# Kernel tuning notes

Hardware: AMD Instinct MI355X
Metric: run time of the kernel (lower is better)

Reference implementation:

```python
import jax, jax.numpy as jnp
import numpy as np

DIM = 512
HEADS = 8
DIM_HEAD = 64
INNER = HEADS * DIM_HEAD  # 512
B, N = 4, 2048


def setup_inputs() -> dict:
    key = jax.random.key(0)
    k1, k2, k3, k4 = jax.random.split(key, 4)
    x = jax.random.normal(k1, (B, N, DIM), dtype=jnp.float32)
    # nn.Linear(dim, inner*3, bias=False): weight [3*inner, dim]; store transposed [dim, 3*inner]
    w_qkv = jax.random.normal(k2, (DIM, 3 * INNER), dtype=jnp.float32) / np.sqrt(DIM)
    w_out = jax.random.normal(k3, (INNER, DIM), dtype=jnp.float32) / np.sqrt(INNER)
    b_out = jax.random.normal(k4, (DIM,), dtype=jnp.float32) * 0.01
    return {"x": x, "w_qkv": w_qkv, "w_out": w_out, "b_out": b_out}


def reference(x, w_qkv, w_out, b_out):
    b, n, _ = x.shape
    scale = DIM_HEAD ** -0.5
    qkv = x @ w_qkv  # [b, n, 3*inner]
    q, k, v = jnp.split(qkv, 3, axis=-1)
    # [b, n, h, d] -> [b, h, n, d]
    reshape = lambda t: t.reshape(b, n, HEADS, DIM_HEAD).transpose(0, 2, 1, 3)
    q, k, v = reshape(q), reshape(k), reshape(v)
    dots = jnp.einsum('bhid,bhjd->bhij', q, k) * scale  # [b, h, n, n]
    attn = jax.nn.softmax(dots, axis=-1)
    out = jnp.einsum('bhij,bhjd->bhid', attn, v)  # [b, h, n, d]
    out = out.transpose(0, 2, 1, 3).reshape(b, n, INNER)
    return out @ w_out + b_out  # dropout is identity at inference
```

## Files before the change

kernel.cpp:

```cpp
#include <hip/hip_runtime.h>
#include <hip/hip_bf16.h>
#include <cstdint>

#define DEV __device__ __forceinline__

typedef __attribute__((ext_vector_type(8))) __bf16 bf16x8;
typedef __attribute__((ext_vector_type(4))) float floatx4;
typedef __attribute__((ext_vector_type(4))) short shortx4;
typedef __attribute__((ext_vector_type(8))) short shortx8;

constexpr float QSCALE = 0.18033688011112042f;

DEV unsigned short f2b(float f) {
  union { float f; unsigned u; } v; v.f = f;
  return (unsigned short)((v.u + 0x7fffu + ((v.u >> 16) & 1u)) >> 16);
}

#if defined(__has_builtin) && __has_builtin(__builtin_amdgcn_cvt_pk_bf16_f32)
DEV unsigned pk2(float a, float b) {
  typedef __attribute__((ext_vector_type(2))) __bf16 bf2;
  union { bf2 v; unsigned u; } u;
  u.v = __builtin_amdgcn_cvt_pk_bf16_f32(a, b);
  return u.u;
}
#else
DEV unsigned pk2(float a, float b) {
  return (unsigned)f2b(a) | ((unsigned)f2b(b) << 16);
}
#endif

#if defined(__has_builtin) && __has_builtin(__builtin_amdgcn_exp2f)
DEV float fexp2(float x) { return __builtin_amdgcn_exp2f(x); }
#else
DEV float fexp2(float x) { return exp2f(x); }
#endif

DEV floatx4 mfma16(bf16x8 a, bf16x8 b, floatx4 c) {
  return __builtin_amdgcn_mfma_f32_16x16x32_bf16(a, b, c, 0, 0, 0);
}

#define GLD_LDS16(gp, lp)                                                          \
  __builtin_amdgcn_global_load_lds(                                                \
      (const __attribute__((address_space(1))) void*)(gp),                         \
      (__attribute__((address_space(3))) void*)(lp), 16, 0, 0)

__global__ void cvt_f32_bf16(const float* __restrict__ in,
                             unsigned short* __restrict__ out, int n4) {
  int i = blockIdx.x * 256 + threadIdx.x;
  if (i >= n4) return;
  floatx4 f = ((const floatx4*)in)[i];
  shortx4 s;
  s[0] = (short)f2b(f[0]); s[1] = (short)f2b(f[1]);
  s[2] = (short)f2b(f[2]); s[3] = (short)f2b(f[3]);
  ((shortx4*)out)[i] = s;
}

__global__ void tcvt(const float* __restrict__ in, unsigned short* __restrict__ out,
                     int R, int C) {
  __shared__ float tile[32][33];
  int tx = threadIdx.x & 31, ty = threadIdx.x >> 5;
  int r0 = blockIdx.y * 32, c0 = blockIdx.x * 32;
#pragma unroll
  for (int i = 0; i < 4; i++) {
    int rr = ty + i * 8;
    tile[rr][tx] = in[(size_t)(r0 + rr) * C + c0 + tx];
  }
  __syncthreads();
#pragma unroll
  for (int i = 0; i < 4; i++) {
    int rr = ty + i * 8;
    out[(size_t)(c0 + rr) * R + r0 + tx] = f2b(tile[tx][rr]);
  }
}

template <int MODE>
__global__ __launch_bounds__(256, 2) void gemm_bt(
    const unsigned short* __restrict__ A, const unsigned short* __restrict__ Bt, int K,
    unsigned short* __restrict__ qg, unsigned short* __restrict__ kg,
    unsigned short* __restrict__ vtg, float* __restrict__ outF,
    const float* __restrict__ bias) {
  __shared__ __align__(16) unsigned short smem[128 * 136];
  unsigned short* Xs = smem;
  unsigned short* Ws = smem + 4096;
  const int tid = threadIdx.x;
  const int lane = tid & 63, wid = tid >> 6;
  const int g = lane >> 4, r = lane & 15;
  const int m0 = blockIdx.y * 128, n0 = blockIdx.x * 128;
  const int wm = (wid & 1) * 64, wn = (wid >> 1) * 64;

  floatx4 acc[4][4] = {};

  const int c0i = tid, c1i = 256 + tid;
  const int row0 = c0i >> 2, kb0 = (c0i & 3) ^ ((row0 >> 1) & 3);
  const int row1 = c1i >> 2, kb1 = (c1i & 3) ^ ((row1 >> 1) & 3);
  const unsigned ldsOff0 = (unsigned)(wid * 64) * 16;
  const unsigned ldsOff1 = (unsigned)(256 + wid * 64) * 16;

  for (int kt = 0; kt < K; kt += 32) {
    GLD_LDS16(A + (size_t)(m0 + row0) * K + kt + kb0 * 8, (char*)Xs + ldsOff0);
    GLD_LDS16(A + (size_t)(m0 + row1) * K + kt + kb1 * 8, (char*)Xs + ldsOff1);
    GLD_LDS16(Bt + (size_t)(n0 + row0) * K + kt + kb0 * 8, (char*)Ws + ldsOff0);
    GLD_LDS16(Bt + (size_t)(n0 + row1) * K + kt + kb1 * 8, (char*)Ws + ldsOff1);
    __syncthreads();
    bf16x8 a[4], b[4];
#pragma unroll
    for (int t = 0; t < 4; t++) {
      int rowA = wm + t * 16 + r;
      a[t] = *(const bf16x8*)(Xs + rowA * 32 + (g ^ ((rowA >> 1) & 3)) * 8);
      int rowB = wn + t * 16 + r;
      b[t] = *(const bf16x8*)(Ws + rowB * 32 + (g ^ ((rowB >> 1) & 3)) * 8);
    }
#pragma unroll
    for (int mt = 0; mt < 4; mt++)
#pragma unroll
      for (int nt = 0; nt < 4; nt++)
        acc[mt][nt] = mfma16(a[mt], b[nt], acc[mt][nt]);
    __syncthreads();
  }

  if (MODE == 0) {
    const int which = blockIdx.x >> 2;
    if (which == 2) {
      const int tokbase = m0 + wm;
      const int bb = tokbase >> 11, nb = tokbase & 2047;
#pragma unroll
      for (int mt = 0; mt < 4; mt++) {
        const int s = (mt >> 1) * 32 + g * 8 + (mt & 1) * 4;
#pragma unroll
        for (int nt = 0; nt < 4; nt++) {
          int vcol = n0 + wn + nt * 16 + r - 1024;
          int h = vcol >> 6, d = vcol & 63;
          unsigned long long w =
              (unsigned long long)pk2(acc[mt][nt][0], acc[mt][nt][1]) |
              ((unsigned long long)pk2(acc[mt][nt][2], acc[mt][nt][3]) << 32);
          *(unsigned long long*)(vtg + ((size_t)(bb * 8 + h) * 64 + d) * 2048 +
                                 nb + s) = w;
        }
      }
    } else {
      const float sc = (which == 0) ? QSCALE : 1.f;
      unsigned short* dst = (which == 0) ? qg : kg;
#pragma unroll
      for (int mt = 0; mt < 4; mt++)
#pragma unroll
        for (int nt = 0; nt < 4; nt++) {
          int col = wn + nt * 16 + r;
#pragma unroll
          for (int e = 0; e < 4; e++) {
            int row = wm + mt * 16 + g * 4 + e;
            smem[row * 136 + col] = f2b(acc[mt][nt][e] * sc);
          }
        }
      __syncthreads();
#pragma unroll
      for (int it = 0; it < 8; it++) {
        int c = it * 256 + tid;
        int row = c >> 4, cc = c & 15;
        shortx8 v = *(const shortx8*)(smem + row * 136 + cc * 8);
        int gq = n0 + cc * 8;
        int h = (gq >> 6) & 7, d0 = gq & 63;
        int tok = m0 + row, bb = tok >> 11, n = tok & 2047;
        *(shortx8*)(dst + ((size_t)(bb * 8 + h) * 2048 + n) * 64 + d0) = v;
      }
    }
  } else {
    float* ftile = (float*)smem;
#pragma unroll
    for (int half = 0; half < 2; half++) {
      if (half) __syncthreads();
#pragma unroll
      for (int mi = 0; mi < 2; mi++) {
        int mt = half * 2 + mi;
#pragma unroll
        for (int nt = 0; nt < 4; nt++)
#pragma unroll
          for (int e = 0; e < 4; e++) {
            int lr = (wm >> 1) + mi * 16 + g * 4 + e;
            ftile[lr * 132 + wn + nt * 16 + r] = acc[mt][nt][e];
          }
      }
      __syncthreads();
#pragma unroll
      for (int it = 0; it < 8; it++) {
        int c = it * 256 + tid;
        int lr = c >> 5, cc = c & 31;
        floatx4 v = *(const floatx4*)(ftile + lr * 132 + cc * 4);
        int col = n0 + cc * 4;
        v += *(const floatx4*)(bias + col);
        int rowt = (lr < 32) ? (half * 32 + lr) : (64 + half * 32 + (lr - 32));
        *(floatx4*)(outF + (size_t)(m0 + rowt) * 512 + col) = v;
      }
    }
  }
}

__global__ __launch_bounds__(256, 1) void attn(
    const unsigned short* __restrict__ qg, const unsigned short* __restrict__ kg,
    const unsigned short* __restrict__ vtg, unsigned short* __restrict__ ao) {
  __shared__ __align__(16) unsigned short Os[4][64 * 72];
  const int tid = threadIdx.x, lane = tid & 63, wid = tid >> 6;
  const int g = lane >> 4, r = lane & 15;
  const int bh = blockIdx.y;
  const int qw = blockIdx.x * 256 + wid * 64;
  const size_t base = (size_t)bh * (2048 * 64);
  const unsigned short* Vb = vtg + base;

  bf16x8 bq[4][2];
#pragma unroll
  for (int nt = 0; nt < 4; nt++)
#pragma unroll
    for (int kc = 0; kc < 2; kc++)
      bq[nt][kc] = *(const bf16x8*)(qg + base + (size_t)(qw + nt * 16 + r) * 64 +
                                    kc * 32 + g * 8);

  bf16x8 vones;
#pragma unroll
  for (int i = 0; i < 8; i++) vones[i] = (__bf16)1.0f;

  floatx4 o[4][4] = {};
  floatx4 lacc[4] = {};

  bf16x8 ak[4][2];
#pragma unroll
  for (int mt = 0; mt < 4; mt++)
#pragma unroll
    for (int kc = 0; kc < 2; kc++)
      ak[mt][kc] = *(const bf16x8*)(kg + base + (size_t)(mt * 16 + r) * 64 +
                                    kc * 32 + g * 8);

  for (int n0 = 0; n0 < 2048; n0 += 64) {
    bf16x8 bv[4][2];
#pragma unroll
    for (int b = 0; b < 4; b++)
#pragma unroll
      for (int kc = 0; kc < 2; kc++)
        bv[b][kc] = *(const bf16x8*)(Vb + (size_t)(b * 16 + r) * 2048 + n0 +
                                     kc * 32 + g * 8);

    floatx4 st[4][4] = {};
#pragma unroll
    for (int kc = 0; kc < 2; kc++)
#pragma unroll
      for (int mt = 0; mt < 4; mt++)
#pragma unroll
        for (int nt = 0; nt < 4; nt++)
          st[mt][nt] = mfma16(ak[mt][kc], bq[nt][kc], st[mt][nt]);

    if (n0 + 64 < 2048) {
#pragma unroll
      for (int mt = 0; mt < 4; mt++)
#pragma unroll
        for (int kc = 0; kc < 2; kc++)
          ak[mt][kc] = *(const bf16x8*)(kg + base +
                                        (size_t)(n0 + 64 + mt * 16 + r) * 64 +
                                        kc * 32 + g * 8);
    }

    bf16x8 ap[4][2];
#pragma unroll
    for (int a = 0; a < 4; a++) {
      float p[4][4];
#pragma unroll
      for (int mt = 0; mt < 4; mt++)
#pragma unroll
        for (int e = 0; e < 4; e++) p[mt][e] = fexp2(st[mt][a][e]);
#pragma unroll
      for (int kc = 0; kc < 2; kc++) {
        union { unsigned u[4]; bf16x8 v; } w;
        w.u[0] = pk2(p[2 * kc][0], p[2 * kc][1]);
        w.u[1] = pk2(p[2 * kc][2], p[2 * kc][3]);
        w.u[2] = pk2(p[2 * kc + 1][0], p[2 * kc + 1][1]);
        w.u[3] = pk2(p[2 * kc + 1][2], p[2 * kc + 1][3]);
        ap[a][kc] = w.v;
      }
    }

#pragma unroll
    for (int kc = 0; kc < 2; kc++) {
#pragma unroll
      for (int a = 0; a < 4; a++) {
        lacc[a] = mfma16(ap[a][kc], vones, lacc[a]);
#pragma unroll
        for (int b = 0; b < 4; b++)
          o[a][b] = mfma16(ap[a][kc], bv[b][kc], o[a][b]);
      }
    }
  }

#pragma unroll
  for (int a = 0; a < 4; a++) {
    floatx4 il;
#pragma unroll
    for (int e = 0; e < 4; e++) il[e] = 1.f / lacc[a][e];
#pragma unroll
    for (int b = 0; b < 4; b++)
#pragma unroll
      for (int e = 0; e < 4; e++)
        Os[wid][(a * 16 + g * 4 + e) * 72 + b * 16 + r] = f2b(o[a][b][e] * il[e]);
  }
  __syncthreads();
  const int bb = bh >> 3, h = bh & 7;
#pragma unroll
  for (int it = 0; it < 8; it++) {
    int c = it * 64 + lane;
    int row = c >> 3, cc = c & 7;
    shortx8 v = *(const shortx8*)(&Os[wid][row * 72 + cc * 8]);
    *(shortx8*)(ao + ((size_t)(bb * 2048 + qw + row)) * 512 + h * 64 + cc * 8) = v;
  }
}

extern "C" void kernel_launch(void* const* d_in, const int* in_sizes, int n_in,
                              void* d_out, int out_size, void* d_ws, size_t ws_size,
                              hipStream_t stream) {
  const float* x = (const float*)d_in[0];
  const float* w_qkv = (const float*)d_in[1];
  const float* w_out = (const float*)d_in[2];
  const float* b_out = (const float*)d_in[3];
  float* out = (float*)d_out;

  unsigned short* wsp = (unsigned short*)d_ws;
  unsigned short* xb = wsp;
  unsigned short* wqkvt = xb + (size_t)8192 * 512;
  unsigned short* woutt = wqkvt + (size_t)1536 * 512;
  unsigned short* qg = woutt + (size_t)512 * 512;
  unsigned short* kg = qg + (size_t)32 * 2048 * 64;
  unsigned short* vtg = kg + (size_t)32 * 2048 * 64;
  unsigned short* ao = vtg + (size_t)32 * 2048 * 64;

  cvt_f32_bf16<<<4096, 256, 0, stream>>>(x, xb, 8192 * 512 / 4);
  tcvt<<<dim3(48, 16), 256, 0, stream>>>(w_qkv, wqkvt, 512, 1536);
  tcvt<<<dim3(16, 16), 256, 0, stream>>>(w_out, woutt, 512, 512);
  gemm_bt<0><<<dim3(12, 64), 256, 0, stream>>>(xb, wqkvt, 512, qg, kg, vtg,
                                               nullptr, nullptr);
  attn<<<dim3(8, 32), 256, 0, stream>>>(qg, kg, vtg, ao);
  gemm_bt<1><<<dim3(4, 64), 256, 0, stream>>>(ao, woutt, 512, nullptr, nullptr,
                                              nullptr, out, b_out);
}
```

Before: 180.6 us.

## Double-buffer GEMM and attention K/V tiles in LDS, split keys across waves

Both GEMMs now double-buffer their LDS tiles, issuing the next k-slice's async global-to-LDS loads before computing on the current one, so each iteration needs one barrier instead of two. The QKV GEMM uses 256-row tiles so each block reuses the weight tile across more rows. Attention now stages K and V^T tiles into swizzled, double-buffered LDS that pairs of waves share. Each block covers 128 queries, with the key range split between wave pairs and their partial sums combined through LDS at the end. This doubles the attention grid and raises occupancy to 2 blocks per CU, at the cost of more LDS, extra barriers and a final cross-wave reduction.

```diff
diff --git a/kernel.cpp b/kernel.cpp
--- a/kernel.cpp
+++ b/kernel.cpp
@@ -73,84 +73,101 @@
   }
 }
 
-template <int MODE>
-__global__ __launch_bounds__(256, 2) void gemm_bt(
-    const unsigned short* __restrict__ A, const unsigned short* __restrict__ Bt, int K,
+__global__ __launch_bounds__(256, 2) void gemm_qkv(
+    const unsigned short* __restrict__ A, const unsigned short* __restrict__ Bt,
     unsigned short* __restrict__ qg, unsigned short* __restrict__ kg,
-    unsigned short* __restrict__ vtg, float* __restrict__ outF,
-    const float* __restrict__ bias) {
-  __shared__ __align__(16) unsigned short smem[128 * 136];
-  unsigned short* Xs = smem;
-  unsigned short* Ws = smem + 4096;
+    unsigned short* __restrict__ vtg) {
+  __shared__ __align__(16) unsigned short smem[24576];
   const int tid = threadIdx.x;
   const int lane = tid & 63, wid = tid >> 6;
   const int g = lane >> 4, r = lane & 15;
-  const int m0 = blockIdx.y * 128, n0 = blockIdx.x * 128;
-  const int wm = (wid & 1) * 64, wn = (wid >> 1) * 64;
-
-  floatx4 acc[4][4] = {};
-
-  const int c0i = tid, c1i = 256 + tid;
-  const int row0 = c0i >> 2, kb0 = (c0i & 3) ^ ((row0 >> 1) & 3);
-  const int row1 = c1i >> 2, kb1 = (c1i & 3) ^ ((row1 >> 1) & 3);
-  const unsigned ldsOff0 = (unsigned)(wid * 64) * 16;
-  const unsigned ldsOff1 = (unsigned)(256 + wid * 64) * 16;
-
-  for (int kt = 0; kt < K; kt += 32) {
-    GLD_LDS16(A + (size_t)(m0 + row0) * K + kt + kb0 * 8, (char*)Xs + ldsOff0);
-    GLD_LDS16(A + (size_t)(m0 + row1) * K + kt + kb1 * 8, (char*)Xs + ldsOff1);
-    GLD_LDS16(Bt + (size_t)(n0 + row0) * K + kt + kb0 * 8, (char*)Ws + ldsOff0);
-    GLD_LDS16(Bt + (size_t)(n0 + row1) * K + kt + kb1 * 8, (char*)Ws + ldsOff1);
+  const int m0 = blockIdx.y * 256, n0 = blockIdx.x * 128;
+  const int wm = (wid & 1) * 128, wn = (wid >> 1) * 64;
+  const int K = 512;
+
+  floatx4 acc[8][4] = {};
+
+  int rowA[4], kbA[4];
+#pragma unroll
+  for (int i = 0; i < 4; i++) {
+    int c = i * 256 + tid;
+    rowA[i] = c >> 2;
+    kbA[i] = (c & 3) ^ ((rowA[i] >> 1) & 3);
+  }
+
+#define STAGE_QKV(kt, b)                                                         \
+  {                                                                              \
+    _Pragma("unroll") for (int i = 0; i < 4; i++)                                \
+        GLD_LDS16(A + (size_t)(m0 + rowA[i]) * K + (kt) + kbA[i] * 8,            \
+                  (char*)smem + (b)*16384 + i * 4096 + wid * 1024);              \
+    _Pragma("unroll") for (int i = 0; i < 2; i++)                                \
+        GLD_LDS16(Bt + (size_t)(n0 + rowA[i]) * K + (kt) + kbA[i] * 8,           \
+                  (char*)smem + 32768 + (b)*8192 + i * 4096 + wid * 1024);       \
+  }
+
+  STAGE_QKV(0, 0)
+  for (int it = 0; it < 16; it++) {
+    const int buf = it & 1;
     __syncthreads();
-    bf16x8 a[4], b[4];
+    if (it + 1 < 16) STAGE_QKV((it + 1) * 32, buf ^ 1)
+    const unsigned short* Xs = smem + buf * 8192;
+    const unsigned short* Ws = smem + 16384 + buf * 4096;
+    bf16x8 a[8], b[4];
+#pragma unroll
+    for (int t = 0; t < 8; t++) {
+      int rw = wm + t * 16 + r;
+      a[t] = *(const bf16x8*)(Xs + rw * 32 + (g ^ ((rw >> 1) & 3)) * 8);
+    }
 #pragma unroll
     for (int t = 0; t < 4; t++) {
-      int rowA = wm + t * 16 + r;
-      a[t] = *(const bf16x8*)(Xs + rowA * 32 + (g ^ ((rowA >> 1) & 3)) * 8);
-      int rowB = wn + t * 16 + r;
-      b[t] = *(const bf16x8*)(Ws + rowB * 32 + (g ^ ((rowB >> 1) & 3)) * 8);
-    }
-#pragma unroll
-    for (int mt = 0; mt < 4; mt++)
+      int rw = wn + t * 16 + r;
+      b[t] = *(const bf16x8*)(Ws + rw * 32 + (g ^ ((rw >> 1) & 3)) * 8);
+    }
+#pragma unroll
+    for (int mt = 0; mt < 8; mt++)
 #pragma unroll
       for (int nt = 0; nt < 4; nt++)
         acc[mt][nt] = mfma16(a[mt], b[nt], acc[mt][nt]);
-    __syncthreads();
-  }
-
-  if (MODE == 0) {
-    const int which = blockIdx.x >> 2;
-    if (which == 2) {
-      const int tokbase = m0 + wm;
-      const int bb = tokbase >> 11, nb = tokbase & 2047;
-#pragma unroll
-      for (int mt = 0; mt < 4; mt++) {
-        const int s = (mt >> 1) * 32 + g * 8 + (mt & 1) * 4;
-#pragma unroll
-        for (int nt = 0; nt < 4; nt++) {
-          int vcol = n0 + wn + nt * 16 + r - 1024;
-          int h = vcol >> 6, d = vcol & 63;
-          unsigned long long w =
-              (unsigned long long)pk2(acc[mt][nt][0], acc[mt][nt][1]) |
-              ((unsigned long long)pk2(acc[mt][nt][2], acc[mt][nt][3]) << 32);
-          *(unsigned long long*)(vtg + ((size_t)(bb * 8 + h) * 64 + d) * 2048 +
-                                 nb + s) = w;
-        }
-      }
-    } else {
-      const float sc = (which == 0) ? QSCALE : 1.f;
-      unsigned short* dst = (which == 0) ? qg : kg;
-#pragma unroll
-      for (int mt = 0; mt < 4; mt++)
-#pragma unroll
-        for (int nt = 0; nt < 4; nt++) {
-          int col = wn + nt * 16 + r;
-#pragma unroll
-          for (int e = 0; e < 4; e++) {
-            int row = wm + mt * 16 + g * 4 + e;
-            smem[row * 136 + col] = f2b(acc[mt][nt][e] * sc);
+  }
+#undef STAGE_QKV
+
+  const int which = blockIdx.x >> 2;
+  if (which == 2) {
+    const int tokbase = m0 + wm;
+    const int bb = tokbase >> 11, nbase = tokbase & 2047;
+#pragma unroll
+    for (int mt = 0; mt < 8; mt++) {
+      const int m3 = mt & 3;
+      const int s = (mt >> 2) * 64 + (m3 >> 1) * 32 + g * 8 + (m3 & 1) * 4;
+#pragma unroll
+      for (int nt = 0; nt < 4; nt++) {
+        int vcol = n0 + wn + nt * 16 + r - 1024;
+        int h = vcol >> 6, d = vcol & 63;
+        unsigned long long w =
+            (unsigned long long)pk2(acc[mt][nt][0], acc[mt][nt][1]) |
+            ((unsigned long long)pk2(acc[mt][nt][2], acc[mt][nt][3]) << 32);
+        *(unsigned long long*)(vtg + ((size_t)(bb * 8 + h) * 64 + d) * 2048 +
+                               nbase + s) = w;
+      }
+    }
+  } else {
+    const float sc = (which == 0) ? QSCALE : 1.f;
+    unsigned short* dst = (which == 0) ? qg : kg;
+#pragma unroll
+    for (int half = 0; half < 2; half++) {
+      __syncthreads();
+      if ((wid & 1) == half) {
+#pragma unroll
+        for (int mt = 0; mt < 8; mt++)
+#pragma unroll
+          for (int nt = 0; nt < 4; nt++) {
+            int rl = mt * 16 + g * 4;
+            int col = wn + nt * 16 + r;
+#pragma unroll
+            for (int e = 0; e < 4; e++)
+              smem[(rl + e) * 136 + col] = f2b(acc[mt][nt][e] * sc);
           }
-        }
+      }
       __syncthreads();
 #pragma unroll
       for (int it = 0; it < 8; it++) {
@@ -159,58 +176,117 @@
         shortx8 v = *(const shortx8*)(smem + row * 136 + cc * 8);
         int gq = n0 + cc * 8;
         int h = (gq >> 6) & 7, d0 = gq & 63;
-        int tok = m0 + row, bb = tok >> 11, n = tok & 2047;
+        int tok = m0 + half * 128 + row, bb = tok >> 11, n = tok & 2047;
         *(shortx8*)(dst + ((size_t)(bb * 8 + h) * 2048 + n) * 64 + d0) = v;
       }
     }
-  } else {
-    float* ftile = (float*)smem;
-#pragma unroll
-    for (int half = 0; half < 2; half++) {
-      if (half) __syncthreads();
-#pragma unroll
-      for (int mi = 0; mi < 2; mi++) {
-        int mt = half * 2 + mi;
-#pragma unroll
-        for (int nt = 0; nt < 4; nt++)
-#pragma unroll
-          for (int e = 0; e < 4; e++) {
-            int lr = (wm >> 1) + mi * 16 + g * 4 + e;
-            ftile[lr * 132 + wn + nt * 16 + r] = acc[mt][nt][e];
-          }
-      }
-      __syncthreads();
-#pragma unroll
-      for (int it = 0; it < 8; it++) {
-        int c = it * 256 + tid;
-        int lr = c >> 5, cc = c & 31;
-        floatx4 v = *(const floatx4*)(ftile + lr * 132 + cc * 4);
-        int col = n0 + cc * 4;
-        v += *(const floatx4*)(bias + col);
-        int rowt = (lr < 32) ? (half * 32 + lr) : (64 + half * 32 + (lr - 32));
-        *(floatx4*)(outF + (size_t)(m0 + rowt) * 512 + col) = v;
-      }
-    }
-  }
-}
-
-__global__ __launch_bounds__(256, 1) void attn(
+  }
+}
+
+__global__ __launch_bounds__(256, 2) void gemm_out(
+    const unsigned short* __restrict__ A, const unsigned short* __restrict__ Bt,
+    float* __restrict__ outF, const float* __restrict__ bias) {
+  __shared__ __align__(16) unsigned short smem[17408];
+  const int tid = threadIdx.x;
+  const int lane = tid & 63, wid = tid >> 6;
+  const int g = lane >> 4, r = lane & 15;
+  const int m0 = blockIdx.y * 128, n0 = blockIdx.x * 128;
+  const int wm = (wid & 1) * 64, wn = (wid >> 1) * 64;
+  const int K = 512;
+
+  floatx4 acc[4][4] = {};
+
+  int rowA[2], kbA[2];
+#pragma unroll
+  for (int i = 0; i < 2; i++) {
+    int c = i * 256 + tid;
+    rowA[i] = c >> 2;
+    kbA[i] = (c & 3) ^ ((rowA[i] >> 1) & 3);
+  }
+
+#define STAGE_OUT(kt, b)                                                         \
+  {                                                                              \
+    _Pragma("unroll") for (int i = 0; i < 2; i++) {                              \
+      GLD_LDS16(A + (size_t)(m0 + rowA[i]) * K + (kt) + kbA[i] * 8,              \
+                (char*)smem + (b)*8192 + i * 4096 + wid * 1024);                 \
+      GLD_LDS16(Bt + (size_t)(n0 + rowA[i]) * K + (kt) + kbA[i] * 8,             \
+                (char*)smem + 16384 + (b)*8192 + i * 4096 + wid * 1024);         \
+    }                                                                            \
+  }
+
+  STAGE_OUT(0, 0)
+  for (int it = 0; it < 16; it++) {
+    const int buf = it & 1;
+    __syncthreads();
+    if (it + 1 < 16) STAGE_OUT((it + 1) * 32, buf ^ 1)
+    const unsigned short* Xs = smem + buf * 4096;
+    const unsigned short* Ws = smem + 8192 + buf * 4096;
+    bf16x8 a[4], b[4];
+#pragma unroll
+    for (int t = 0; t < 4; t++) {
+      int rw = wm + t * 16 + r;
+      a[t] = *(const bf16x8*)(Xs + rw * 32 + (g ^ ((rw >> 1) & 3)) * 8);
+      int rb = wn + t * 16 + r;
+      b[t] = *(const bf16x8*)(Ws + rb * 32 + (g ^ ((rb >> 1) & 3)) * 8);
+    }
+#pragma unroll
+    for (int mt = 0; mt < 4; mt++)
+#pragma unroll
+      for (int nt = 0; nt < 4; nt++)
+        acc[mt][nt] = mfma16(a[mt], b[nt], acc[mt][nt]);
+  }
+#undef STAGE_OUT
+
+  float* ftile = (float*)smem;
+#pragma unroll
+  for (int half = 0; half < 2; half++) {
+    __syncthreads();
+#pragma unroll
+    for (int mi = 0; mi < 2; mi++) {
+      int mt = half * 2 + mi;
+#pragma unroll
+      for (int nt = 0; nt < 4; nt++)
+#pragma unroll
+        for (int e = 0; e < 4; e++) {
+          int lr = (wm >> 1) + mi * 16 + g * 4 + e;
+          ftile[lr * 132 + wn + nt * 16 + r] = acc[mt][nt][e];
+        }
+    }
+    __syncthreads();
+#pragma unroll
+    for (int it = 0; it < 8; it++) {
+      int c = it * 256 + tid;
+      int lr = c >> 5, cc = c & 31;
+      floatx4 v = *(const floatx4*)(ftile + lr * 132 + cc * 4);
+      int col = n0 + cc * 4;
+      v += *(const floatx4*)(bias + col);
+      int rowt = (lr < 32) ? (half * 32 + lr) : (64 + half * 32 + (lr - 32));
+      *(floatx4*)(outF + (size_t)(m0 + rowt) * 512 + col) = v;
+    }
+  }
+}
+
+__global__ __launch_bounds__(256, 2) void attn(
     const unsigned short* __restrict__ qg, const unsigned short* __restrict__ kg,
     const unsigned short* __restrict__ vtg, unsigned short* __restrict__ ao) {
-  __shared__ __align__(16) unsigned short Os[4][64 * 72];
+  __shared__ __align__(16) char L[65536];
+  unsigned short* Ksm = (unsigned short*)L;
+  unsigned short* Vtm = (unsigned short*)(L + 32768);
   const int tid = threadIdx.x, lane = tid & 63, wid = tid >> 6;
-  const int g = lane >> 4, r = lane & 15;
+  const int g = lane >> 4, r = lane & 15, r7 = r & 7;
+  const int wq = wid & 1, wk = wid >> 1;
   const int bh = blockIdx.y;
-  const int qw = blockIdx.x * 256 + wid * 64;
+  const int q0 = blockIdx.x * 128 + wq * 64;
   const size_t base = (size_t)bh * (2048 * 64);
-  const unsigned short* Vb = vtg + base;
+  const int chunk = (lane & 7) ^ ((lane >> 3) & 7);
+  const int srow = lane >> 3;
 
   bf16x8 bq[4][2];
 #pragma unroll
   for (int nt = 0; nt < 4; nt++)
 #pragma unroll
     for (int kc = 0; kc < 2; kc++)
-      bq[nt][kc] = *(const bf16x8*)(qg + base + (size_t)(qw + nt * 16 + r) * 64 +
+      bq[nt][kc] = *(const bf16x8*)(qg + base + (size_t)(q0 + nt * 16 + r) * 64 +
                                     kc * 32 + g * 8);
 
   bf16x8 vones;
@@ -220,41 +296,39 @@
   floatx4 o[4][4] = {};
   floatx4 lacc[4] = {};
 
-  bf16x8 ak[4][2];
-#pragma unroll
-  for (int mt = 0; mt < 4; mt++)
+#define STAGE_ATTN(it, b)                                                        \
+  {                                                                              \
+    const int sn0 = (it)*128 + wk * 64;                                          \
+    if (wq == 0) {                                                               \
+      _Pragma("unroll") for (int j = 0; j < 8; j++)                              \
+          GLD_LDS16(kg + base + (size_t)(sn0 + j * 8 + srow) * 64 + chunk * 8,   \
+                    (char*)L + ((b)*2 + wk) * 8192 + j * 1024);                  \
+    } else {                                                                     \
+      _Pragma("unroll") for (int j = 0; j < 8; j++)                              \
+          GLD_LDS16(vtg + base + (size_t)(j * 8 + srow) * 2048 + sn0 + chunk * 8,\
+                    (char*)L + 32768 + ((b)*2 + wk) * 8192 + j * 1024);          \
+    }                                                                            \
+  }
+
+  STAGE_ATTN(0, 0)
+  for (int it = 0; it < 16; it++) {
+    const int buf = it & 1;
+    __syncthreads();
+    if (it + 1 < 16) STAGE_ATTN(it + 1, buf ^ 1)
+    const unsigned short* Kt = Ksm + (buf * 2 + wk) * 4096;
+    const unsigned short* Vt = Vtm + (buf * 2 + wk) * 4096;
+
+    floatx4 st[4][4] = {};
 #pragma unroll
     for (int kc = 0; kc < 2; kc++)
-      ak[mt][kc] = *(const bf16x8*)(kg + base + (size_t)(mt * 16 + r) * 64 +
-                                    kc * 32 + g * 8);
-
-  for (int n0 = 0; n0 < 2048; n0 += 64) {
-    bf16x8 bv[4][2];
-#pragma unroll
-    for (int b = 0; b < 4; b++)
-#pragma unroll
-      for (int kc = 0; kc < 2; kc++)
-        bv[b][kc] = *(const bf16x8*)(Vb + (size_t)(b * 16 + r) * 2048 + n0 +
-                                     kc * 32 + g * 8);
-
-    floatx4 st[4][4] = {};
-#pragma unroll
-    for (int kc = 0; kc < 2; kc++)
-#pragma unroll
-      for (int mt = 0; mt < 4; mt++)
+#pragma unroll
+      for (int mt = 0; mt < 4; mt++) {
+        bf16x8 ak = *(const bf16x8*)(Kt + (mt * 16 + r) * 64 +
+                                     ((kc * 4 + g) ^ r7) * 8);
 #pragma unroll
         for (int nt = 0; nt < 4; nt++)
-          st[mt][nt] = mfma16(ak[mt][kc], bq[nt][kc], st[mt][nt]);
-
-    if (n0 + 64 < 2048) {
-#pragma unroll
-      for (int mt = 0; mt < 4; mt++)
-#pragma unroll
-        for (int kc = 0; kc < 2; kc++)
-          ak[mt][kc] = *(const bf16x8*)(kg + base +
-                                        (size_t)(n0 + 64 + mt * 16 + r) * 64 +
-                                        kc * 32 + g * 8);
-    }
+          st[mt][nt] = mfma16(ak, bq[nt][kc], st[mt][nt]);
+      }
 
     bf16x8 ap[4][2];
 #pragma unroll
@@ -277,35 +351,64 @@
 
 #pragma unroll
     for (int kc = 0; kc < 2; kc++) {
+      bf16x8 bv[4];
+#pragma unroll
+      for (int b = 0; b < 4; b++)
+        bv[b] = *(const bf16x8*)(Vt + (b * 16 + r) * 64 +
+                                 ((kc * 4 + g) ^ r7) * 8);
 #pragma unroll
       for (int a = 0; a < 4; a++) {
         lacc[a] = mfma16(ap[a][kc], vones, lacc[a]);
 #pragma unroll
         for (int b = 0; b < 4; b++)
-          o[a][b] = mfma16(ap[a][kc], bv[b][kc], o[a][b]);
-      }
-    }
-  }
-
-#pragma unroll
-  for (int a = 0; a < 4; a++) {
-    floatx4 il;
-#pragma unroll
-    for (int e = 0; e < 4; e++) il[e] = 1.f / lacc[a][e];
-#pragma unroll
-    for (int b = 0; b < 4; b++)
-#pragma unroll
-      for (int e = 0; e < 4; e++)
-        Os[wid][(a * 16 + g * 4 + e) * 72 + b * 16 + r] = f2b(o[a][b][e] * il[e]);
+          o[a][b] = mfma16(ap[a][kc], bv[b], o[a][b]);
+      }
+    }
+  }
+#undef STAGE_ATTN
+
+  float* fP = (float*)L;
+  float* fL = (float*)(L + 32768);
+  unsigned short* Osm = (unsigned short*)(L + 40960);
+  __syncthreads();
+  if (wk == 1) {
+#pragma unroll
+    for (int a = 0; a < 4; a++) {
+      *(floatx4*)&fL[wq * 1024 + a * 256 + lane * 4] = lacc[a];
+#pragma unroll
+      for (int b = 0; b < 4; b++)
+        *(floatx4*)&fP[wq * 4096 + (a * 4 + b) * 256 + lane * 4] = o[a][b];
+    }
+  }
+  __syncthreads();
+  if (wk == 0) {
+#pragma unroll
+    for (int a = 0; a < 4; a++) {
+      floatx4 lt = lacc[a] + *(floatx4*)&fL[wq * 1024 + a * 256 + lane * 4];
+      floatx4 il;
+#pragma unroll
+      for (int e = 0; e < 4; e++) il[e] = 1.f / lt[e];
+#pragma unroll
+      for (int b = 0; b < 4; b++) {
+        floatx4 oo = o[a][b] +
+                     *(floatx4*)&fP[wq * 4096 + (a * 4 + b) * 256 + lane * 4];
+#pragma unroll
+        for (int e = 0; e < 4; e++)
+          Osm[wq * 4608 + (a * 16 + g * 4 + e) * 72 + b * 16 + r] =
+              f2b(oo[e] * il[e]);
+      }
+    }
   }
   __syncthreads();
   const int bb = bh >> 3, h = bh & 7;
 #pragma unroll
-  for (int it = 0; it < 8; it++) {
-    int c = it * 64 + lane;
+  for (int it = 0; it < 4; it++) {
+    int c = it * 256 + tid;
     int row = c >> 3, cc = c & 7;
-    shortx8 v = *(const shortx8*)(&Os[wid][row * 72 + cc * 8]);
-    *(shortx8*)(ao + ((size_t)(bb * 2048 + qw + row)) * 512 + h * 64 + cc * 8) = v;
+    int wqi = row >> 6, r6 = row & 63;
+    shortx8 v = *(const shortx8*)(Osm + wqi * 4608 + r6 * 72 + cc * 8);
+    int tok = blockIdx.x * 128 + row;
+    *(shortx8*)(ao + ((size_t)(bb * 2048 + tok)) * 512 + h * 64 + cc * 8) = v;
   }
 }
 
@@ -330,9 +433,7 @@
   cvt_f32_bf16<<<4096, 256, 0, stream>>>(x, xb, 8192 * 512 / 4);
   tcvt<<<dim3(48, 16), 256, 0, stream>>>(w_qkv, wqkvt, 512, 1536);
   tcvt<<<dim3(16, 16), 256, 0, stream>>>(w_out, woutt, 512, 512);
-  gemm_bt<0><<<dim3(12, 64), 256, 0, stream>>>(xb, wqkvt, 512, qg, kg, vtg,
-                                               nullptr, nullptr);
-  attn<<<dim3(8, 32), 256, 0, stream>>>(qg, kg, vtg, ao);
-  gemm_bt<1><<<dim3(4, 64), 256, 0, stream>>>(ao, woutt, 512, nullptr, nullptr,
-                                              nullptr, out, b_out);
-}
+  gemm_qkv<<<dim3(12, 32), 256, 0, stream>>>(xb, wqkvt, qg, kg, vtg);
+  attn<<<dim3(16, 32), 256, 0, stream>>>(qg, kg, vtg, ao);
+  gemm_out<<<dim3(4, 64), 256, 0, stream>>>(ao, woutt, out, b_out);
+}
```

Result: faster. 157.7 us (-12.7%).
